# Kernel tuning notes

Hardware: AMD Instinct MI355X
Metric: run time of the kernel (lower is better)

The kernel has to match this reference:

```python
import jax, jax.numpy as jnp
import numpy as np

N_QUBITS = 6
N_LAYERS = 2
FEATURE_DIMS = [768, 512, 1024]
BATCH = 16384
PI = np.float32(np.pi)
C64 = jnp.complex64


def _ry(t):
    c = jnp.cos(t / 2).astype(C64)
    s = jnp.sin(t / 2).astype(C64)
    return jnp.stack([jnp.stack([c, -s], -1), jnp.stack([s, c], -1)], -2)


def _rx(t):
    c = jnp.cos(t / 2).astype(C64)
    s = (-1j * jnp.sin(t / 2).astype(C64))
    return jnp.stack([jnp.stack([c, s], -1), jnp.stack([s, c], -1)], -2)


def _rz(t):
    e = jnp.exp(-0.5j * t.astype(C64))
    z = jnp.zeros_like(e)
    return jnp.stack([jnp.stack([e, z], -1), jnp.stack([z, jnp.conj(e)], -1)], -2)


def _apply_1q(state, gate, wire):
    # state: [B, 2,...,2]; gate: [2,2] (shared) or [B,2,2] (per-sample)
    s = jnp.moveaxis(state, wire + 1, -1)
    shp = s.shape
    s = s.reshape(shp[0], -1, 2)
    if gate.ndim == 2:
        s = jnp.einsum('ij,bkj->bki', gate, s)
    else:
        s = jnp.einsum('bij,bkj->bki', gate, s)
    return jnp.moveaxis(s.reshape(shp), -1, wire + 1)


def _apply_cnot(state, control, target):
    s = jnp.moveaxis(state, (control + 1, target + 1), (1, 2))
    s = jnp.stack([s[:, 0], s[:, 1, ::-1]], axis=1)
    return jnp.moveaxis(s, (1, 2), (control + 1, target + 1))


def _apply_cry(state, theta, control, target):
    s = jnp.moveaxis(state, (control + 1, target + 1), (1, 2))
    g = _ry(theta)  # [2,2]
    c1 = jnp.einsum('ij,bj...->bi...', g, s[:, 1])
    s = jnp.stack([s[:, 0], c1], axis=1)
    return jnp.moveaxis(s, (1, 2), (control + 1, target + 1))


def run_circuit(angles, qw):
    # angles: [B, n_qubits] encoding RY angles; qw: [n_layers, n_qubits, 3]
    B = angles.shape[0]
    n = N_QUBITS
    state = jnp.zeros((B,) + (2,) * n, C64).at[(slice(None),) + (0,) * n].set(1.0)
    # encoding: sequential RYs on a wire compose to RY(sum of angles); RY(0) is identity
    for i in range(n):
        state = _apply_1q(state, _ry(angles[:, i]), i)
    for l in range(N_LAYERS):
        for i in range(n):
            state = _apply_1q(state, _rx(qw[l, i, 0]), i)
            state = _apply_1q(state, _ry(qw[l, i, 1]), i)
            state = _apply_1q(state, _rz(qw[l, i, 2]), i)
        for i in range(n - 1):
            state = _apply_cnot(state, i, i + 1)
        if n > 2:
            state = _apply_cnot(state, 0, n - 1)
        for i in range(0, n - 1, 2):
            state = _apply_cry(state, qw[l, i, 1], i, i + 1)
    probs = state.real ** 2 + state.imag ** 2  # [B, 2,...,2]
    z = [(jnp.take(probs, 0, axis=i + 1) - jnp.take(probs, 1, axis=i + 1)).reshape(B, -1).sum(-1)
         for i in range(n)]
    return jnp.stack(z, axis=-1)  # [B, n_qubits]


def setup_inputs() -> dict:
    key = jax.random.key(0)
    ks = jax.random.split(key, 10)
    inp = {}
    for m, d in enumerate(FEATURE_DIMS):
        inp[f'feat{m}'] = jax.random.normal(ks[m], (BATCH, d), jnp.float32)
        inp[f'W{m}'] = jax.random.normal(ks[3 + m], (d, N_QUBITS), jnp.float32) / np.sqrt(d)
        inp[f'b{m}'] = jnp.zeros((N_QUBITS,), jnp.float32)
    inp['qw'] = 0.1 * jax.random.normal(ks[6], (N_LAYERS, N_QUBITS, 3), jnp.float32)
    inp['fusion_logits'] = jnp.ones((len(FEATURE_DIMS),), jnp.float32) / len(FEATURE_DIMS)
    return inp


def reference(feat0, feat1, feat2, W0, b0, W1, b1, W2, b2, qw, fusion_logits):
    fw = jax.nn.softmax(fusion_logits)
    q0 = jnp.tanh(feat0 @ W0 + b0)  # [B, n_qubits]
    q1 = jnp.tanh(feat1 @ W1 + b1)
    q2 = jnp.tanh(feat2 @ W2 + b2)
    angles = PI * (fw[0] * q0 + fw[1] * q1 + fw[2] * q2)
    return run_circuit(angles, qw)
```

## Files before the change

### kernel.cpp

```cpp
#include <hip/hip_runtime.h>

#define PI_F 3.14159265358979323846f

#define WT0_OFF 0
#define WT1_OFF 4608
#define WT2_OFF 7680
#define WT_FLOATS 13824

__global__ void wt_kernel(const float* __restrict__ W0, const float* __restrict__ W1,
                          const float* __restrict__ W2, float* __restrict__ wt) {
    int t = blockIdx.x * 256 + threadIdx.x;
    if (t < 4608) {
        int j = t / 768, k = t - j * 768;
        wt[WT0_OFF + t] = W0[k * 6 + j];
    } else if (t < 7680) {
        int u = t - 4608; int j = u / 512, k = u - j * 512;
        wt[WT1_OFF + u] = W1[k * 6 + j];
    } else if (t < WT_FLOATS) {
        int u = t - 7680; int j = u / 1024, k = u - j * 1024;
        wt[WT2_OFF + u] = W2[k * 6 + j];
    }
}


template<int CTRL>
__device__ __forceinline__ float dppmov(float v) {
    return __int_as_float(__builtin_amdgcn_update_dpp(0, __float_as_int(v), CTRL, 0xF, 0xF, true));
}
template<int PAT>
__device__ __forceinline__ float swzf(float v) {
    return __int_as_float(__builtin_amdgcn_ds_swizzle(__float_as_int(v), PAT));
}

template<int M>
__device__ __forceinline__ float xsh(float v) {
    if constexpr (M == 1)       return dppmov<0xB1>(v);
    else if constexpr (M == 2)  return dppmov<0x4E>(v);
    else if constexpr (M == 4)  return swzf<0x101F>(v);
    else if constexpr (M == 8)  return dppmov<0x128>(v);
    else if constexpr (M == 16) return swzf<0x401F>(v);
    else                        return __shfl_xor(v, 32, 64);
}

__device__ __forceinline__ float pl16_sum(float v) {
#if __has_builtin(__builtin_amdgcn_permlane16_swap)
    auto r = __builtin_amdgcn_permlane16_swap(__float_as_uint(v), __float_as_uint(v), false, false);
    return __uint_as_float(r[0]) + __uint_as_float(r[1]);
#else
    return v + swzf<0x401F>(v);
#endif
}
__device__ __forceinline__ float pl32_sum(float v) {
#if __has_builtin(__builtin_amdgcn_permlane32_swap)
    auto r = __builtin_amdgcn_permlane32_swap(__float_as_uint(v), __float_as_uint(v), false, false);
    return __uint_as_float(r[0]) + __uint_as_float(r[1]);
#else
    return v + __shfl_xor(v, 32, 64);
#endif
}

__device__ __forceinline__ float bfly_sum(float v) {
    v += dppmov<0xB1>(v);
    v += dppmov<0x4E>(v);
    v += swzf<0x101F>(v);
    v += dppmov<0x128>(v);
    v = pl16_sum(v);
    v = pl32_sum(v);
    return v;
}

__device__ __forceinline__ float fast_tanh(float x) {
    float e = __expf(2.0f * x);
    return 1.0f - 2.0f / (e + 1.0f);
}


template<int D>
__device__ __forceinline__ void gemv2(const float* __restrict__ f, const float* __restrict__ wt,
                                      int lane, float acc[2][6]) {
    constexpr int CH = D / 256;
    constexpr int RD = D / 4;
    const float4* __restrict__ x0 = (const float4*)f;
    const float4* __restrict__ x1 = (const float4*)(f + D);
    const float4* __restrict__ w4 = (const float4*)wt;
    float4 a0 = x0[lane];
    float4 a1 = x1[lane];
#pragma unroll
    for (int j = 0; j < 6; ++j) { acc[0][j] = 0.0f; acc[1][j] = 0.0f; }
#pragma unroll
    for (int ch = 0; ch < CH; ++ch) {
        float4 n0 = a0, n1 = a1;
        if (ch + 1 < CH) {
            n0 = x0[(ch + 1) * 64 + lane];
            n1 = x1[(ch + 1) * 64 + lane];
        }
#pragma unroll
        for (int j = 0; j < 6; ++j) {
            float4 w = w4[j * RD + ch * 64 + lane];
            acc[0][j] = fmaf(a0.x, w.x, fmaf(a0.y, w.y, fmaf(a0.z, w.z, fmaf(a0.w, w.w, acc[0][j]))));
            acc[1][j] = fmaf(a1.x, w.x, fmaf(a1.y, w.y, fmaf(a1.z, w.z, fmaf(a1.w, w.w, acc[1][j]))));
        }
        a0 = n0; a1 = n1;
    }
}


template<int M>
__device__ __forceinline__ void gateU(float (&re)[2], float (&im)[2], int lane,
                                      float ar, float ai, float br, float bi) {
    const bool hi = (lane & M) != 0;
    const float Ai = hi ? -ai : ai;
    const float Br = hi ? -br : br;
#pragma unroll
    for (int s = 0; s < 2; ++s) {
        float pre = xsh<M>(re[s]);
        float pim = xsh<M>(im[s]);
        float nr = ar * re[s] - Ai * im[s] + Br * pre - bi * pim;
        float ni = ar * im[s] + Ai * re[s] + Br * pim + bi * pre;
        re[s] = nr; im[s] = ni;
    }
}

template<int MC, int MT>
__device__ __forceinline__ void gateCNOT(float (&re)[2], float (&im)[2], int lane) {
    const bool c1 = (lane & MC) != 0;
#pragma unroll
    for (int s = 0; s < 2; ++s) {
        float pre = xsh<MT>(re[s]);
        float pim = xsh<MT>(im[s]);
        re[s] = c1 ? pre : re[s];
        im[s] = c1 ? pim : im[s];
    }
}

template<int MC, int MT>
__device__ __forceinline__ void gateCRY(float (&re)[2], float (&im)[2], int lane, float c, float sn) {
    const bool c1 = (lane & MC) != 0;
    const float sg = (lane & MT) ? sn : -sn;
#pragma unroll
    for (int s = 0; s < 2; ++s) {
        float pre = xsh<MT>(re[s]);
        float pim = xsh<MT>(im[s]);
        float nr = fmaf(c, re[s], sg * pre);
        float ni = fmaf(c, im[s], sg * pim);
        re[s] = c1 ? nr : re[s];
        im[s] = c1 ? ni : im[s];
    }
}

template<int L, int I>
__device__ __forceinline__ void rotLayer(float (&re)[2], float (&im)[2], int lane,
                                         const float* __restrict__ qw) {
    constexpr int M = 32 >> I;
    constexpr int G = (L * 6 + I) * 3;
    float a = qw[G + 0], b = qw[G + 1], g = qw[G + 2];
    float ca, sa, cb, sb, cc, sc;
    __sincosf(0.5f * a, &sa, &ca);
    __sincosf(0.5f * b, &sb, &cb);
    __sincosf(0.5f * g, &sc, &cc);
    float m00r = cb * ca, m00i = sb * sa;
    float m01r = -sb * ca, m01i = -cb * sa;
    float u00r = m00r * cc + m00i * sc, u00i = m00i * cc - m00r * sc;
    float u01r = m01r * cc + m01i * sc, u01i = m01i * cc - m01r * sc;
    gateU<M>(re, im, lane, u00r, u00i, u01r, u01i);
}

template<int L, int I>
__device__ __forceinline__ void cryLayer(float (&re)[2], float (&im)[2], int lane,
                                         const float* __restrict__ qw) {
    constexpr int MC = 32 >> I;
    constexpr int MT = 16 >> I;
    float c, sn;
    __sincosf(0.5f * qw[(L * 6 + I) * 3 + 1], &sn, &c);
    gateCRY<MC, MT>(re, im, lane, c, sn);
}


#define D0 768
#define D1 512
#define D2 1024

__global__ __launch_bounds__(256, 6) void qf_main(
    const float* __restrict__ f0, const float* __restrict__ b0,
    const float* __restrict__ f1, const float* __restrict__ b1,
    const float* __restrict__ f2, const float* __restrict__ b2,
    const float* __restrict__ qw, const float* __restrict__ fl,
    const float* __restrict__ wt, float* __restrict__ out)
{
    const int lane = threadIdx.x & 63;
    const int wave = blockIdx.x * 4 + (threadIdx.x >> 6);
    const int s0 = wave * 2;

    float l0 = fl[0], l1 = fl[1], l2 = fl[2];
    float mx = fmaxf(l0, fmaxf(l1, l2));
    float e0 = __expf(l0 - mx), e1 = __expf(l1 - mx), e2 = __expf(l2 - mx);
    float inv = 1.0f / (e0 + e1 + e2);
    float fw0 = e0 * inv, fw1 = e1 * inv, fw2 = e2 * inv;

    float acc[2][6], ang[2][6];

    gemv2<D0>(f0 + (size_t)s0 * D0, wt + WT0_OFF, lane, acc);
#pragma unroll
    for (int s = 0; s < 2; ++s)
#pragma unroll
        for (int j = 0; j < 6; ++j)
            ang[s][j] = fw0 * fast_tanh(bfly_sum(acc[s][j]) + b0[j]);

    gemv2<D1>(f1 + (size_t)s0 * D1, wt + WT1_OFF, lane, acc);
#pragma unroll
    for (int s = 0; s < 2; ++s)
#pragma unroll
        for (int j = 0; j < 6; ++j)
            ang[s][j] += fw1 * fast_tanh(bfly_sum(acc[s][j]) + b1[j]);

    gemv2<D2>(f2 + (size_t)s0 * D2, wt + WT2_OFF, lane, acc);
#pragma unroll
    for (int s = 0; s < 2; ++s)
#pragma unroll
        for (int j = 0; j < 6; ++j)
            ang[s][j] = PI_F * (ang[s][j] + fw2 * fast_tanh(bfly_sum(acc[s][j]) + b2[j]));

    float re[2], im[2];
#pragma unroll
    for (int s = 0; s < 2; ++s) {
        float amp = 1.0f;
#pragma unroll
        for (int i = 0; i < 6; ++i) {
            float c, sn;
            __sincosf(0.5f * ang[s][i], &sn, &c);
            amp *= (lane & (32 >> i)) ? sn : c;
        }
        re[s] = amp;
        im[s] = 0.0f;
    }

    rotLayer<0,0>(re, im, lane, qw); rotLayer<0,1>(re, im, lane, qw); rotLayer<0,2>(re, im, lane, qw);
    rotLayer<0,3>(re, im, lane, qw); rotLayer<0,4>(re, im, lane, qw); rotLayer<0,5>(re, im, lane, qw);
    gateCNOT<32,16>(re, im, lane); gateCNOT<16,8>(re, im, lane); gateCNOT<8,4>(re, im, lane);
    gateCNOT<4,2>(re, im, lane);  gateCNOT<2,1>(re, im, lane);  gateCNOT<32,1>(re, im, lane);
    cryLayer<0,0>(re, im, lane, qw); cryLayer<0,2>(re, im, lane, qw); cryLayer<0,4>(re, im, lane, qw);

    rotLayer<1,0>(re, im, lane, qw); rotLayer<1,1>(re, im, lane, qw); rotLayer<1,2>(re, im, lane, qw);
    rotLayer<1,3>(re, im, lane, qw); rotLayer<1,4>(re, im, lane, qw); rotLayer<1,5>(re, im, lane, qw);
    gateCNOT<32,16>(re, im, lane); gateCNOT<16,8>(re, im, lane); gateCNOT<8,4>(re, im, lane);
    gateCNOT<4,2>(re, im, lane);  gateCNOT<2,1>(re, im, lane);  gateCNOT<32,1>(re, im, lane);
    cryLayer<1,0>(re, im, lane, qw); cryLayer<1,2>(re, im, lane, qw); cryLayer<1,4>(re, im, lane, qw);

#pragma unroll
    for (int s = 0; s < 2; ++s) {
        float p = fmaf(re[s], re[s], im[s] * im[s]);
        float q;
        q = xsh<1>(p);  p = (lane & 1)  ? (q - p) : (p + q);
        q = xsh<2>(p);  p = (lane & 2)  ? (q - p) : (p + q);
        q = xsh<4>(p);  p = (lane & 4)  ? (q - p) : (p + q);
        q = xsh<8>(p);  p = (lane & 8)  ? (q - p) : (p + q);
        q = xsh<16>(p); p = (lane & 16) ? (q - p) : (p + q);
        q = xsh<32>(p); p = (lane & 32) ? (q - p) : (p + q);
        if (__popc(lane) == 1)
            out[(size_t)(s0 + s) * 6 + (6 - __ffs(lane))] = p;
    }
}

extern "C" void kernel_launch(void* const* d_in, const int* in_sizes, int n_in,
                              void* d_out, int out_size, void* d_ws, size_t ws_size,
                              hipStream_t stream) {
    const float* f0 = (const float*)d_in[0];
    const float* W0 = (const float*)d_in[1];
    const float* b0 = (const float*)d_in[2];
    const float* f1 = (const float*)d_in[3];
    const float* W1 = (const float*)d_in[4];
    const float* b1 = (const float*)d_in[5];
    const float* f2 = (const float*)d_in[6];
    const float* W2 = (const float*)d_in[7];
    const float* b2 = (const float*)d_in[8];
    const float* qw = (const float*)d_in[9];
    const float* fl = (const float*)d_in[10];
    float* out = (float*)d_out;
    float* wt = (float*)d_ws;

    wt_kernel<<<54, 256, 0, stream>>>(W0, W1, W2, wt);
    qf_main<<<2048, 256, 0, stream>>>(f0, b0, f1, b1, f2, b2, qw, fl, wt, out);
}
```

Measured before the change: 53.13 us.

## Precompute gate matrices, fold encoding into first rotation layer, issue all feature loads upfront

A prep kernel now also computes the fused RX·RY·RZ unitaries and CRY cos/sin once, so they are no longer recomputed per wave. In the main kernel, the first rotation layer is folded analytically into the product-state construction, and each CNOT chain is replaced by a single permutation shuffle. All feature rows are loaded into registers before any compute to expose memory-level parallelism, and launch bounds are relaxed to allow the extra registers. The cost is higher register pressure and lower occupancy, which may reduce latency hiding on this memory-bound GEMV.

```diff
diff --git a/kernel.cpp b/kernel.cpp
--- a/kernel.cpp
+++ b/kernel.cpp
@@ -2,23 +2,47 @@
 
 #define PI_F 3.14159265358979323846f
 
-#define WT0_OFF 0
-#define WT1_OFF 4608
-#define WT2_OFF 7680
+#define D0 768
+#define D1 512
+#define D2 1024
 #define WT_FLOATS 13824
-
-__global__ void wt_kernel(const float* __restrict__ W0, const float* __restrict__ W1,
-                          const float* __restrict__ W2, float* __restrict__ wt) {
+#define U_OFF   WT_FLOATS
+#define CRY_OFF (WT_FLOATS + 48)
+
+
+__global__ void prep_kernel(const float* __restrict__ W0, const float* __restrict__ W1,
+                            const float* __restrict__ W2, const float* __restrict__ qw,
+                            float* __restrict__ ws) {
     int t = blockIdx.x * 256 + threadIdx.x;
     if (t < 4608) {
         int j = t / 768, k = t - j * 768;
-        wt[WT0_OFF + t] = W0[k * 6 + j];
+        ws[t] = W0[k * 6 + j];
     } else if (t < 7680) {
-        int u = t - 4608; int j = u / 512, k = u - j * 512;
-        wt[WT1_OFF + u] = W1[k * 6 + j];
+        int u = t - 4608, j = u / 512, k = u - j * 512;
+        ws[t] = W1[k * 6 + j];
     } else if (t < WT_FLOATS) {
-        int u = t - 7680; int j = u / 1024, k = u - j * 1024;
-        wt[WT2_OFF + u] = W2[k * 6 + j];
+        int u = t - 7680, j = u / 1024, k = u - j * 1024;
+        ws[t] = W2[k * 6 + j];
+    } else if (t < WT_FLOATS + 12) {
+        int g = t - WT_FLOATS;
+        float ca, sa, cb, sb, cc, sc;
+        sincosf(0.5f * qw[g * 3 + 0], &sa, &ca);
+        sincosf(0.5f * qw[g * 3 + 1], &sb, &cb);
+        sincosf(0.5f * qw[g * 3 + 2], &sc, &cc);
+        float m00r = cb * ca, m00i = sb * sa;
+        float m01r = -sb * ca, m01i = -cb * sa;
+        float* u4 = ws + U_OFF + g * 4;
+        u4[0] = m00r * cc + m00i * sc;
+        u4[1] = m00i * cc - m00r * sc;
+        u4[2] = m01r * cc + m01i * sc;
+        u4[3] = m01i * cc - m01r * sc;
+    } else if (t < WT_FLOATS + 18) {
+        int k = t - WT_FLOATS - 12;
+        int l = k / 3, i = (k - l * 3) * 2;
+        float c, s;
+        sincosf(0.5f * qw[(l * 6 + i) * 3 + 1], &s, &c);
+        ws[CRY_OFF + k * 2 + 0] = c;
+        ws[CRY_OFF + k * 2 + 1] = s;
     }
 }
 
@@ -74,34 +98,8 @@
     return 1.0f - 2.0f / (e + 1.0f);
 }
 
-
-template<int D>
-__device__ __forceinline__ void gemv2(const float* __restrict__ f, const float* __restrict__ wt,
-                                      int lane, float acc[2][6]) {
-    constexpr int CH = D / 256;
-    constexpr int RD = D / 4;
-    const float4* __restrict__ x0 = (const float4*)f;
-    const float4* __restrict__ x1 = (const float4*)(f + D);
-    const float4* __restrict__ w4 = (const float4*)wt;
-    float4 a0 = x0[lane];
-    float4 a1 = x1[lane];
-#pragma unroll
-    for (int j = 0; j < 6; ++j) { acc[0][j] = 0.0f; acc[1][j] = 0.0f; }
-#pragma unroll
-    for (int ch = 0; ch < CH; ++ch) {
-        float4 n0 = a0, n1 = a1;
-        if (ch + 1 < CH) {
-            n0 = x0[(ch + 1) * 64 + lane];
-            n1 = x1[(ch + 1) * 64 + lane];
-        }
-#pragma unroll
-        for (int j = 0; j < 6; ++j) {
-            float4 w = w4[j * RD + ch * 64 + lane];
-            acc[0][j] = fmaf(a0.x, w.x, fmaf(a0.y, w.y, fmaf(a0.z, w.z, fmaf(a0.w, w.w, acc[0][j]))));
-            acc[1][j] = fmaf(a1.x, w.x, fmaf(a1.y, w.y, fmaf(a1.z, w.z, fmaf(a1.w, w.w, acc[1][j]))));
-        }
-        a0 = n0; a1 = n1;
-    }
+__device__ __forceinline__ float dot4(float4 a, float4 w, float acc) {
+    return fmaf(a.x, w.x, fmaf(a.y, w.y, fmaf(a.z, w.z, fmaf(a.w, w.w, acc))));
 }
 
 
@@ -118,18 +116,6 @@
         float nr = ar * re[s] - Ai * im[s] + Br * pre - bi * pim;
         float ni = ar * im[s] + Ai * re[s] + Br * pim + bi * pre;
         re[s] = nr; im[s] = ni;
-    }
-}
-
-template<int MC, int MT>
-__device__ __forceinline__ void gateCNOT(float (&re)[2], float (&im)[2], int lane) {
-    const bool c1 = (lane & MC) != 0;
-#pragma unroll
-    for (int s = 0; s < 2; ++s) {
-        float pre = xsh<MT>(re[s]);
-        float pim = xsh<MT>(im[s]);
-        re[s] = c1 ? pre : re[s];
-        im[s] = c1 ? pim : im[s];
     }
 }
 
@@ -148,48 +134,77 @@
     }
 }
 
-template<int L, int I>
-__device__ __forceinline__ void rotLayer(float (&re)[2], float (&im)[2], int lane,
-                                         const float* __restrict__ qw) {
+template<int I>
+__device__ __forceinline__ void l1gate(float (&re)[2], float (&im)[2], int lane,
+                                       const float* __restrict__ ws) {
     constexpr int M = 32 >> I;
-    constexpr int G = (L * 6 + I) * 3;
-    float a = qw[G + 0], b = qw[G + 1], g = qw[G + 2];
-    float ca, sa, cb, sb, cc, sc;
-    __sincosf(0.5f * a, &sa, &ca);
-    __sincosf(0.5f * b, &sb, &cb);
-    __sincosf(0.5f * g, &sc, &cc);
-    float m00r = cb * ca, m00i = sb * sa;
-    float m01r = -sb * ca, m01i = -cb * sa;
-    float u00r = m00r * cc + m00i * sc, u00i = m00i * cc - m00r * sc;
-    float u01r = m01r * cc + m01i * sc, u01i = m01i * cc - m01r * sc;
-    gateU<M>(re, im, lane, u00r, u00i, u01r, u01i);
-}
-
-template<int L, int I>
-__device__ __forceinline__ void cryLayer(float (&re)[2], float (&im)[2], int lane,
-                                         const float* __restrict__ qw) {
-    constexpr int MC = 32 >> I;
-    constexpr int MT = 16 >> I;
-    float c, sn;
-    __sincosf(0.5f * qw[(L * 6 + I) * 3 + 1], &sn, &c);
-    gateCRY<MC, MT>(re, im, lane, c, sn);
-}
-
-
-#define D0 768
-#define D1 512
-#define D2 1024
-
-__global__ __launch_bounds__(256, 6) void qf_main(
+    const float ar = ws[U_OFF + (6 + I) * 4 + 0];
+    const float ai = ws[U_OFF + (6 + I) * 4 + 1];
+    const float br = ws[U_OFF + (6 + I) * 4 + 2];
+    const float bi = ws[U_OFF + (6 + I) * 4 + 3];
+    gateU<M>(re, im, lane, ar, ai, br, bi);
+}
+
+template<int L, int P>
+__device__ __forceinline__ void cryGate(float (&re)[2], float (&im)[2], int lane,
+                                        const float* __restrict__ ws) {
+    constexpr int MC = 32 >> (2 * P);
+    constexpr int MT = 16 >> (2 * P);
+    const float c = ws[CRY_OFF + (L * 3 + P) * 2 + 0];
+    const float s = ws[CRY_OFF + (L * 3 + P) * 2 + 1];
+    gateCRY<MC, MT>(re, im, lane, c, s);
+}
+
+__device__ __forceinline__ void buildState(const float (&ang)[6], int lane,
+                                           const float* __restrict__ ws,
+                                           float& reO, float& imO) {
+    float pr, pi;
+#pragma unroll
+    for (int i = 0; i < 6; ++i) {
+        float cq, sq;
+        __sincosf(0.5f * ang[i], &sq, &cq);
+        const float ar = ws[U_OFF + i * 4 + 0];
+        const float ai = ws[U_OFF + i * 4 + 1];
+        const float br = ws[U_OFF + i * 4 + 2];
+        const float bi = ws[U_OFF + i * 4 + 3];
+        float vloR = ar * cq + br * sq;
+        float vloI = ai * cq + bi * sq;
+        float vhiR = ar * sq - br * cq;
+        float vhiI = bi * cq - ai * sq;
+        bool hi = (lane & (32 >> i)) != 0;
+        float vr = hi ? vhiR : vloR;
+        float vi = hi ? vhiI : vloI;
+        if (i == 0) { pr = vr; pi = vi; }
+        else { float t = pr * vr - pi * vi; pi = pr * vi + pi * vr; pr = t; }
+    }
+    reO = pr; imO = pi;
+}
+
+
+__global__ __launch_bounds__(256, 3) void qf_main(
     const float* __restrict__ f0, const float* __restrict__ b0,
     const float* __restrict__ f1, const float* __restrict__ b1,
     const float* __restrict__ f2, const float* __restrict__ b2,
-    const float* __restrict__ qw, const float* __restrict__ fl,
-    const float* __restrict__ wt, float* __restrict__ out)
+    const float* __restrict__ fl, const float* __restrict__ ws,
+    float* __restrict__ out)
 {
     const int lane = threadIdx.x & 63;
     const int wave = blockIdx.x * 4 + (threadIdx.x >> 6);
     const int s0 = wave * 2;
+
+    const float4* __restrict__ xA0 = (const float4*)(f0 + (size_t)s0 * D0);
+    const float4* __restrict__ xB0 = (const float4*)(f0 + (size_t)(s0 + 1) * D0);
+    const float4* __restrict__ xA1 = (const float4*)(f1 + (size_t)s0 * D1);
+    const float4* __restrict__ xB1 = (const float4*)(f1 + (size_t)(s0 + 1) * D1);
+    const float4* __restrict__ xA2 = (const float4*)(f2 + (size_t)s0 * D2);
+    const float4* __restrict__ xB2 = (const float4*)(f2 + (size_t)(s0 + 1) * D2);
+
+    float4 xa0 = xA0[lane], xa1 = xA0[64 + lane], xa2 = xA0[128 + lane];
+    float4 xb0 = xB0[lane], xb1 = xB0[64 + lane], xb2 = xB0[128 + lane];
+    float4 xa3 = xA1[lane], xa4 = xA1[64 + lane];
+    float4 xb3 = xB1[lane], xb4 = xB1[64 + lane];
+    float4 xa5 = xA2[lane], xa6 = xA2[64 + lane], xa7 = xA2[128 + lane], xa8 = xA2[192 + lane];
+    float4 xb5 = xB2[lane], xb6 = xB2[64 + lane], xb7 = xB2[128 + lane], xb8 = xB2[192 + lane];
 
     float l0 = fl[0], l1 = fl[1], l2 = fl[2];
     float mx = fmaxf(l0, fmaxf(l1, l2));
@@ -197,54 +212,73 @@
     float inv = 1.0f / (e0 + e1 + e2);
     float fw0 = e0 * inv, fw1 = e1 * inv, fw2 = e2 * inv;
 
-    float acc[2][6], ang[2][6];
-
-    gemv2<D0>(f0 + (size_t)s0 * D0, wt + WT0_OFF, lane, acc);
-#pragma unroll
-    for (int s = 0; s < 2; ++s)
-#pragma unroll
-        for (int j = 0; j < 6; ++j)
-            ang[s][j] = fw0 * fast_tanh(bfly_sum(acc[s][j]) + b0[j]);
-
-    gemv2<D1>(f1 + (size_t)s0 * D1, wt + WT1_OFF, lane, acc);
-#pragma unroll
-    for (int s = 0; s < 2; ++s)
-#pragma unroll
-        for (int j = 0; j < 6; ++j)
-            ang[s][j] += fw1 * fast_tanh(bfly_sum(acc[s][j]) + b1[j]);
-
-    gemv2<D2>(f2 + (size_t)s0 * D2, wt + WT2_OFF, lane, acc);
-#pragma unroll
-    for (int s = 0; s < 2; ++s)
-#pragma unroll
-        for (int j = 0; j < 6; ++j)
-            ang[s][j] = PI_F * (ang[s][j] + fw2 * fast_tanh(bfly_sum(acc[s][j]) + b2[j]));
+    const float4* __restrict__ w4 = (const float4*)ws;
+    float accA[6], accB[6];
+    float angA[6], angB[6];
+
+#pragma unroll
+    for (int j = 0; j < 6; ++j) {
+        float4 w0 = w4[j * 192 + lane];
+        float4 w1 = w4[j * 192 + 64 + lane];
+        float4 w2 = w4[j * 192 + 128 + lane];
+        float a = 0.f, b = 0.f;
+        a = dot4(xa0, w0, a); a = dot4(xa1, w1, a); a = dot4(xa2, w2, a);
+        b = dot4(xb0, w0, b); b = dot4(xb1, w1, b); b = dot4(xb2, w2, b);
+        accA[j] = a; accB[j] = b;
+    }
+#pragma unroll
+    for (int j = 0; j < 6; ++j) {
+        angA[j] = fw0 * fast_tanh(bfly_sum(accA[j]) + b0[j]);
+        angB[j] = fw0 * fast_tanh(bfly_sum(accB[j]) + b0[j]);
+    }
+
+#pragma unroll
+    for (int j = 0; j < 6; ++j) {
+        float4 w0 = w4[1152 + j * 128 + lane];
+        float4 w1 = w4[1152 + j * 128 + 64 + lane];
+        float a = 0.f, b = 0.f;
+        a = dot4(xa3, w0, a); a = dot4(xa4, w1, a);
+        b = dot4(xb3, w0, b); b = dot4(xb4, w1, b);
+        accA[j] = a; accB[j] = b;
+    }
+#pragma unroll
+    for (int j = 0; j < 6; ++j) {
+        angA[j] += fw1 * fast_tanh(bfly_sum(accA[j]) + b1[j]);
+        angB[j] += fw1 * fast_tanh(bfly_sum(accB[j]) + b1[j]);
+    }
+
+#pragma unroll
+    for (int j = 0; j < 6; ++j) {
+        float4 w0 = w4[1920 + j * 256 + lane];
+        float4 w1 = w4[1920 + j * 256 + 64 + lane];
+        float4 w2 = w4[1920 + j * 256 + 128 + lane];
+        float4 w3 = w4[1920 + j * 256 + 192 + lane];
+        float a = 0.f, b = 0.f;
+        a = dot4(xa5, w0, a); a = dot4(xa6, w1, a); a = dot4(xa7, w2, a); a = dot4(xa8, w3, a);
+        b = dot4(xb5, w0, b); b = dot4(xb6, w1, b); b = dot4(xb7, w2, b); b = dot4(xb8, w3, b);
+        accA[j] = a; accB[j] = b;
+    }
+#pragma unroll
+    for (int j = 0; j < 6; ++j) {
+        angA[j] = PI_F * (angA[j] + fw2 * fast_tanh(bfly_sum(accA[j]) + b2[j]));
+        angB[j] = PI_F * (angB[j] + fw2 * fast_tanh(bfly_sum(accB[j]) + b2[j]));
+    }
+
+    const int sigma = lane ^ ((lane >> 1) & 0x1F) ^ ((lane >> 5) & 1);
 
     float re[2], im[2];
-#pragma unroll
-    for (int s = 0; s < 2; ++s) {
-        float amp = 1.0f;
-#pragma unroll
-        for (int i = 0; i < 6; ++i) {
-            float c, sn;
-            __sincosf(0.5f * ang[s][i], &sn, &c);
-            amp *= (lane & (32 >> i)) ? sn : c;
-        }
-        re[s] = amp;
-        im[s] = 0.0f;
-    }
-
-    rotLayer<0,0>(re, im, lane, qw); rotLayer<0,1>(re, im, lane, qw); rotLayer<0,2>(re, im, lane, qw);
-    rotLayer<0,3>(re, im, lane, qw); rotLayer<0,4>(re, im, lane, qw); rotLayer<0,5>(re, im, lane, qw);
-    gateCNOT<32,16>(re, im, lane); gateCNOT<16,8>(re, im, lane); gateCNOT<8,4>(re, im, lane);
-    gateCNOT<4,2>(re, im, lane);  gateCNOT<2,1>(re, im, lane);  gateCNOT<32,1>(re, im, lane);
-    cryLayer<0,0>(re, im, lane, qw); cryLayer<0,2>(re, im, lane, qw); cryLayer<0,4>(re, im, lane, qw);
-
-    rotLayer<1,0>(re, im, lane, qw); rotLayer<1,1>(re, im, lane, qw); rotLayer<1,2>(re, im, lane, qw);
-    rotLayer<1,3>(re, im, lane, qw); rotLayer<1,4>(re, im, lane, qw); rotLayer<1,5>(re, im, lane, qw);
-    gateCNOT<32,16>(re, im, lane); gateCNOT<16,8>(re, im, lane); gateCNOT<8,4>(re, im, lane);
-    gateCNOT<4,2>(re, im, lane);  gateCNOT<2,1>(re, im, lane);  gateCNOT<32,1>(re, im, lane);
-    cryLayer<1,0>(re, im, lane, qw); cryLayer<1,2>(re, im, lane, qw); cryLayer<1,4>(re, im, lane, qw);
+    buildState(angA, lane, ws, re[0], im[0]);
+    buildState(angB, lane, ws, re[1], im[1]);
+
+    re[0] = __shfl(re[0], sigma, 64); im[0] = __shfl(im[0], sigma, 64);
+    re[1] = __shfl(re[1], sigma, 64); im[1] = __shfl(im[1], sigma, 64);
+    cryGate<0,0>(re, im, lane, ws); cryGate<0,1>(re, im, lane, ws); cryGate<0,2>(re, im, lane, ws);
+
+    l1gate<0>(re, im, lane, ws); l1gate<1>(re, im, lane, ws); l1gate<2>(re, im, lane, ws);
+    l1gate<3>(re, im, lane, ws); l1gate<4>(re, im, lane, ws); l1gate<5>(re, im, lane, ws);
+    re[0] = __shfl(re[0], sigma, 64); im[0] = __shfl(im[0], sigma, 64);
+    re[1] = __shfl(re[1], sigma, 64); im[1] = __shfl(im[1], sigma, 64);
+    cryGate<1,0>(re, im, lane, ws); cryGate<1,1>(re, im, lane, ws); cryGate<1,2>(re, im, lane, ws);
 
 #pragma unroll
     for (int s = 0; s < 2; ++s) {
@@ -276,8 +310,8 @@
     const float* qw = (const float*)d_in[9];
     const float* fl = (const float*)d_in[10];
     float* out = (float*)d_out;
-    float* wt = (float*)d_ws;
-
-    wt_kernel<<<54, 256, 0, stream>>>(W0, W1, W2, wt);
-    qf_main<<<2048, 256, 0, stream>>>(f0, b0, f1, b1, f2, b2, qw, fl, wt, out);
-}
+    float* ws = (float*)d_ws;
+
+    prep_kernel<<<55, 256, 0, stream>>>(W0, W1, W2, qw, ws);
+    qf_main<<<2048, 256, 0, stream>>>(f0, b0, f1, b1, f2, b2, fl, ws, out);
+}
```

Measured after the change: 48.37 us. -9.0%, faster.
